# Performance work log

Hardware: AMD Instinct MI355X
Metric: run time of the kernel (lower is better)

## Reference

```python
import jax, jax.numpy as jnp
import numpy as np

K, B, T, D = 4, 4096, 32, 128


def setup_inputs() -> dict:
    key = jax.random.key(0)
    k1, k2, k3 = jax.random.split(key, 3)
    semb = jax.random.normal(k1, (K, B, D), dtype=jnp.float32)
    slabels = jax.random.randint(k2, (K, B), 0, 2, dtype=jnp.int32)
    topk_ngh = jax.random.randint(k3, (K, B, T), 0, B, dtype=jnp.int32)
    return {"semb": semb, "slabels": slabels, "topk_ngh": topk_ngh}


def reference(semb, slabels, topk_ngh):
    """Dense, masked reformulation of DistanceLayer.forward (hardest=False).

    Original emits, per domain k and anchor i, one triplet for every pair
    (sn, dn) where sn/dn are topk neighbors of i with same/different binary
    label, carrying sim[i,sn] (pos_dist), sim[i,dn] (neg_dist) and the anchor/
    pos/neg embeddings. Here we return the same quantities densified over the
    fixed [K,B,T,T] pair grid with a validity mask (jit-compatible shapes).
    Anchor embeddings are semb itself; pos/neg embeddings are rows of
    nbr_embed selected by the same/diff sides of pair_mask.
    """
    gather = jax.vmap(lambda tbl, idx: tbl[idx])  # per-domain row gather
    nbr_embed = gather(semb, topk_ngh)            # [K,B,T,D]
    nbr_label = gather(slabels, topk_ngh)         # [K,B,T]
    # sim[i, ngh[i,t]] without materializing the full [B,B] sim matrix
    nsim = jnp.einsum('kbd,kbtd->kbt', semb, nbr_embed)  # [K,B,T]
    same = nbr_label == slabels[:, :, None]       # neighbor shares anchor label
    pair_mask = same[:, :, :, None] & (~same)[:, :, None, :]  # [K,B,T,T]
    pos_dist = jnp.where(pair_mask, nsim[:, :, :, None], 0.0)  # sim(i, sn)
    neg_dist = jnp.where(pair_mask, nsim[:, :, None, :], 0.0)  # sim(i, dn)
    return pos_dist, neg_dist, pair_mask, nbr_embed
```

## Files before the change

### kernel.cpp

```cpp
#include <hip/hip_runtime.h>
#include <hip/hip_bf16.h>

constexpr int K = 4;
constexpr int B = 4096;
constexpr int T = 32;
constexpr int D = 128;
constexpr int TT = T * T;
constexpr int TD = T * D;

typedef float f4 __attribute__((ext_vector_type(4)));

__device__ __forceinline__ float dot4(f4 a, f4 b) {
    return a.x * b.x + a.y * b.y + a.z * b.z + a.w * b.w;
}

__device__ __forceinline__ float hreduce32(float p) {
    #pragma unroll
    for (int m = 16; m >= 1; m >>= 1) p += __shfl_xor(p, m, 64);
    return p;
}

__global__ __launch_bounds__(256) void distance_layer_kernel(
    const float* __restrict__ semb,
    const int*   __restrict__ slabels,
    const int*   __restrict__ topk,
    float* __restrict__ pos,
    float* __restrict__ neg,
    float* __restrict__ maskf,
    float* __restrict__ nbr)
{
    const int kb  = blockIdx.x;
    const int k   = kb >> 12;
    const int tid = threadIdx.x;

    __shared__ f4    anchor4[T];
    __shared__ int   idx_s[T];
    __shared__ float nsim_s[T];
    __shared__ int   same_s[T];

    const int my_label = slabels[kb];
    if (tid < T) {
        const int idx = topk[kb * T + tid];
        idx_s[tid]  = idx;
        same_s[tid] = (slabels[(k << 12) + idx] == my_label) ? 1 : 0;
        anchor4[tid] =
            reinterpret_cast<const f4*>(semb + (size_t)kb * D)[tid];
    }
    __syncthreads();

    const f4* semb4 = reinterpret_cast<const f4*>(semb + (size_t)k * B * D);
    f4*       nbr4  = reinterpret_cast<f4*>(nbr + (size_t)kb * TD);

    const int w  = tid >> 5;
    const int d4 = tid & 31;
    const f4  a  = anchor4[d4];
    const int i0 = idx_s[w], i1 = idx_s[8 + w], i2 = idx_s[16 + w], i3 = idx_s[24 + w];

    const f4 s0 = semb4[(size_t)i0 * (D / 4) + d4];
    const f4 s1 = semb4[(size_t)i1 * (D / 4) + d4];
    const f4 s2 = semb4[(size_t)i2 * (D / 4) + d4];
    const f4 s3 = semb4[(size_t)i3 * (D / 4) + d4];
    nbr4[(0  + w) * (D / 4) + d4] = s0;
    nbr4[(8  + w) * (D / 4) + d4] = s1;
    nbr4[(16 + w) * (D / 4) + d4] = s2;
    nbr4[(24 + w) * (D / 4) + d4] = s3;

    const float p0 = hreduce32(dot4(a, s0));
    const float p1 = hreduce32(dot4(a, s1));
    const float p2 = hreduce32(dot4(a, s2));
    const float p3 = hreduce32(dot4(a, s3));
    if (d4 == 0) {
        nsim_s[0  + w] = p0;
        nsim_s[8  + w] = p1;
        nsim_s[16 + w] = p2;
        nsim_s[24 + w] = p3;
    }
    __syncthreads();

    f4* pos4  = reinterpret_cast<f4*>(pos   + (size_t)kb * TT);
    f4* neg4  = reinterpret_cast<f4*>(neg   + (size_t)kb * TT);
    f4* mask4 = reinterpret_cast<f4*>(maskf + (size_t)kb * TT);

    const int s_row = tid >> 3;
    const int d0    = (tid & 7) * 4;
    const int   ss = same_s[s_row];
    const float ps = nsim_s[s_row];

    f4 pv, nv, mv;
    {
        const int m0 = ss & (same_s[d0 + 0] ^ 1);
        const int m1 = ss & (same_s[d0 + 1] ^ 1);
        const int m2 = ss & (same_s[d0 + 2] ^ 1);
        const int m3 = ss & (same_s[d0 + 3] ^ 1);
        pv.x = m0 ? ps : 0.0f;  nv.x = m0 ? nsim_s[d0 + 0] : 0.0f;  mv.x = (float)m0;
        pv.y = m1 ? ps : 0.0f;  nv.y = m1 ? nsim_s[d0 + 1] : 0.0f;  mv.y = (float)m1;
        pv.z = m2 ? ps : 0.0f;  nv.z = m2 ? nsim_s[d0 + 2] : 0.0f;  mv.z = (float)m2;
        pv.w = m3 ? ps : 0.0f;  nv.w = m3 ? nsim_s[d0 + 3] : 0.0f;  mv.w = (float)m3;
    }
    pos4[tid]  = pv;
    neg4[tid]  = nv;
    mask4[tid] = mv;
}

extern "C" void kernel_launch(void* const* d_in, const int* in_sizes, int n_in,
                              void* d_out, int out_size, void* d_ws, size_t ws_size,
                              hipStream_t stream) {
    const float* semb    = (const float*)d_in[0];
    const int*   slabels = (const int*)d_in[1];
    const int*   topk    = (const int*)d_in[2];

    float* out = (float*)d_out;
    const size_t KBTT = (size_t)K * B * T * T;
    float* pos   = out;
    float* neg   = out + KBTT;
    float* maskf = out + 2 * KBTT;
    float* nbr   = out + 3 * KBTT;

    distance_layer_kernel<<<dim3(K * B), dim3(256), 0, stream>>>(
        semb, slabels, topk, pos, neg, maskf, nbr);
}
```

Baseline: 460.4 us.

## Split into metadata kernel and flat streaming writer over output regions

The fused per-anchor kernel becomes two kernels. The first computes per-anchor neighbor similarities, indices and a same-label bitmask into workspace. The second walks the whole output as one flat f4 array, with each block writing a contiguous 2048-vector chunk of a single region (pos, neg, mask or gathered neighbor rows). The aim is long contiguous store streams per block instead of four interleaved scattered regions. In exchange it adds a kernel launch, a workspace round-trip, and reads semb twice (once for the dot products, once for the neighbor copy).

After: 505.6 us. 9.8% more time.

```diff
diff --git a/kernel.cpp b/kernel.cpp
--- a/kernel.cpp
+++ b/kernel.cpp
@@ -7,6 +7,14 @@
 constexpr int D = 128;
 constexpr int TT = T * T;
 constexpr int TD = T * D;
+
+constexpr int META = 80;
+
+constexpr size_t REG_F4   = (size_t)K * B * TT / 4;
+constexpr size_t NBR_BASE = 3 * REG_F4;
+constexpr size_t TOT_F4   = NBR_BASE + (size_t)K * B * TD / 4;
+constexpr int    BLK_F4   = 2048;
+constexpr int    NBLOCKS  = (int)(TOT_F4 / BLK_F4);
 
 typedef float f4 __attribute__((ext_vector_type(4)));
 
@@ -20,14 +28,11 @@
     return p;
 }
 
-__global__ __launch_bounds__(256) void distance_layer_kernel(
+__global__ __launch_bounds__(256) void k_meta(
     const float* __restrict__ semb,
     const int*   __restrict__ slabels,
     const int*   __restrict__ topk,
-    float* __restrict__ pos,
-    float* __restrict__ neg,
-    float* __restrict__ maskf,
-    float* __restrict__ nbr)
+    float* __restrict__ ws)
 {
     const int kb  = blockIdx.x;
     const int k   = kb >> 12;
@@ -36,21 +41,20 @@
     __shared__ f4    anchor4[T];
     __shared__ int   idx_s[T];
     __shared__ float nsim_s[T];
-    __shared__ int   same_s[T];
 
     const int my_label = slabels[kb];
+    int same = 0;
     if (tid < T) {
         const int idx = topk[kb * T + tid];
-        idx_s[tid]  = idx;
-        same_s[tid] = (slabels[(k << 12) + idx] == my_label) ? 1 : 0;
+        idx_s[tid] = idx;
+        same = (slabels[(k << 12) + idx] == my_label) ? 1 : 0;
         anchor4[tid] =
             reinterpret_cast<const f4*>(semb + (size_t)kb * D)[tid];
     }
+    const unsigned long long bal = __ballot(same);
     __syncthreads();
 
     const f4* semb4 = reinterpret_cast<const f4*>(semb + (size_t)k * B * D);
-    f4*       nbr4  = reinterpret_cast<f4*>(nbr + (size_t)kb * TD);
-
     const int w  = tid >> 5;
     const int d4 = tid & 31;
     const f4  a  = anchor4[d4];
@@ -60,10 +64,6 @@
     const f4 s1 = semb4[(size_t)i1 * (D / 4) + d4];
     const f4 s2 = semb4[(size_t)i2 * (D / 4) + d4];
     const f4 s3 = semb4[(size_t)i3 * (D / 4) + d4];
-    nbr4[(0  + w) * (D / 4) + d4] = s0;
-    nbr4[(8  + w) * (D / 4) + d4] = s1;
-    nbr4[(16 + w) * (D / 4) + d4] = s2;
-    nbr4[(24 + w) * (D / 4) + d4] = s3;
 
     const float p0 = hreduce32(dot4(a, s0));
     const float p1 = hreduce32(dot4(a, s1));
@@ -77,29 +77,92 @@
     }
     __syncthreads();
 
-    f4* pos4  = reinterpret_cast<f4*>(pos   + (size_t)kb * TT);
-    f4* neg4  = reinterpret_cast<f4*>(neg   + (size_t)kb * TT);
-    f4* mask4 = reinterpret_cast<f4*>(maskf + (size_t)kb * TT);
+    float* m = ws + (size_t)kb * META;
+    if (tid < T) {
+        m[tid] = nsim_s[tid];
+        reinterpret_cast<int*>(m)[T + tid] = idx_s[tid];
+    }
+    if (tid == 32)
+        reinterpret_cast<unsigned*>(m)[2 * T] = (unsigned)bal;
+}
 
-    const int s_row = tid >> 3;
-    const int d0    = (tid & 7) * 4;
-    const int   ss = same_s[s_row];
-    const float ps = nsim_s[s_row];
+__global__ __launch_bounds__(256) void k_stream(
+    const float* __restrict__ semb,
+    const float* __restrict__ ws,
+    f4* __restrict__ out4)
+{
+    const int tid = threadIdx.x;
+    const size_t g0 = (size_t)blockIdx.x * BLK_F4;
 
-    f4 pv, nv, mv;
-    {
-        const int m0 = ss & (same_s[d0 + 0] ^ 1);
-        const int m1 = ss & (same_s[d0 + 1] ^ 1);
-        const int m2 = ss & (same_s[d0 + 2] ^ 1);
-        const int m3 = ss & (same_s[d0 + 3] ^ 1);
-        pv.x = m0 ? ps : 0.0f;  nv.x = m0 ? nsim_s[d0 + 0] : 0.0f;  mv.x = (float)m0;
-        pv.y = m1 ? ps : 0.0f;  nv.y = m1 ? nsim_s[d0 + 1] : 0.0f;  mv.y = (float)m1;
-        pv.z = m2 ? ps : 0.0f;  nv.z = m2 ? nsim_s[d0 + 2] : 0.0f;  mv.z = (float)m2;
-        pv.w = m3 ? ps : 0.0f;  nv.w = m3 ? nsim_s[d0 + 3] : 0.0f;  mv.w = (float)m3;
+    if (g0 >= NBR_BASE) {
+        const size_t n0 = g0 - NBR_BASE;
+        const f4* semb4 = reinterpret_cast<const f4*>(semb);
+        #pragma unroll
+        for (int i = 0; i < 8; ++i) {
+            const size_t n  = n0 + i * 256 + tid;
+            const int    kb = (int)(n >> 10);
+            const int    q  = (int)(n & 1023);
+            const int    t  = q >> 5;
+            const int    d4 = q & 31;
+            const int idx = reinterpret_cast<const int*>(ws + (size_t)kb * META)[T + t];
+            const int k   = kb >> 12;
+            const f4 v = semb4[(((size_t)(k << 12) + idx) * (D / 4)) + d4];
+            out4[NBR_BASE + n] = v;
+        }
+        return;
     }
-    pos4[tid]  = pv;
-    neg4[tid]  = nv;
-    mask4[tid] = mv;
+
+    const int    region = (int)(g0 / REG_F4);
+    const size_t p0     = g0 % REG_F4;
+    const int    kb0    = (int)(p0 >> 8);
+    const int    s_row  = tid >> 3;
+    const int    dq     = tid & 7;
+
+    if (region == 0) {
+        #pragma unroll
+        for (int i = 0; i < 8; ++i) {
+            const float* m = ws + (size_t)(kb0 + i) * META;
+            const unsigned bits = reinterpret_cast<const unsigned*>(m)[2 * T];
+            const int ss = (bits >> s_row) & 1;
+            const unsigned ndb = ~(bits >> (dq * 4));
+            const float ps = m[s_row];
+            f4 v;
+            v.x = (ss & (ndb & 1))        ? ps : 0.0f;
+            v.y = (ss & ((ndb >> 1) & 1)) ? ps : 0.0f;
+            v.z = (ss & ((ndb >> 2) & 1)) ? ps : 0.0f;
+            v.w = (ss & ((ndb >> 3) & 1)) ? ps : 0.0f;
+            out4[g0 + i * 256 + tid] = v;
+        }
+    } else if (region == 1) {
+        #pragma unroll
+        for (int i = 0; i < 8; ++i) {
+            const float* m = ws + (size_t)(kb0 + i) * META;
+            const unsigned bits = reinterpret_cast<const unsigned*>(m)[2 * T];
+            const int ss = (bits >> s_row) & 1;
+            const unsigned ndb = ~(bits >> (dq * 4));
+            const f4 nd = reinterpret_cast<const f4*>(m)[dq];
+            f4 v;
+            v.x = (ss & (ndb & 1))        ? nd.x : 0.0f;
+            v.y = (ss & ((ndb >> 1) & 1)) ? nd.y : 0.0f;
+            v.z = (ss & ((ndb >> 2) & 1)) ? nd.z : 0.0f;
+            v.w = (ss & ((ndb >> 3) & 1)) ? nd.w : 0.0f;
+            out4[g0 + i * 256 + tid] = v;
+        }
+    } else {
+        #pragma unroll
+        for (int i = 0; i < 8; ++i) {
+            const float* m = ws + (size_t)(kb0 + i) * META;
+            const unsigned bits = reinterpret_cast<const unsigned*>(m)[2 * T];
+            const int ss = (bits >> s_row) & 1;
+            const unsigned ndb = ~(bits >> (dq * 4));
+            f4 v;
+            v.x = (float)(ss & (ndb & 1));
+            v.y = (float)(ss & ((ndb >> 1) & 1));
+            v.z = (float)(ss & ((ndb >> 2) & 1));
+            v.w = (float)(ss & ((ndb >> 3) & 1));
+            out4[g0 + i * 256 + tid] = v;
+        }
+    }
 }
 
 extern "C" void kernel_launch(void* const* d_in, const int* in_sizes, int n_in,
@@ -108,14 +171,9 @@
     const float* semb    = (const float*)d_in[0];
     const int*   slabels = (const int*)d_in[1];
     const int*   topk    = (const int*)d_in[2];
+    float*       ws      = (float*)d_ws;
 
-    float* out = (float*)d_out;
-    const size_t KBTT = (size_t)K * B * T * T;
-    float* pos   = out;
-    float* neg   = out + KBTT;
-    float* maskf = out + 2 * KBTT;
-    float* nbr   = out + 3 * KBTT;
-
-    distance_layer_kernel<<<dim3(K * B), dim3(256), 0, stream>>>(
-        semb, slabels, topk, pos, neg, maskf, nbr);
+    k_meta<<<dim3(K * B), dim3(256), 0, stream>>>(semb, slabels, topk, ws);
+    k_stream<<<dim3(NBLOCKS), dim3(256), 0, stream>>>(
+        semb, ws, reinterpret_cast<f4*>(d_out));
 }
```
